# Optimization experiments

Measured on AMD Instinct MI355X. Metric: run time of the kernel, lower is better.

Reference implementation:

```python
import jax, jax.numpy as jnp
import numpy as np

T, B, X, F, Z, H = 64, 512, 784, 64, 64, 512


def _lin(v, W, b):
    return v @ W.T + b


def _gru(xt, h, Wih, Whh, bih, bhh):
    # PyTorch GRUCell gate math
    gi = xt @ Wih.T + bih
    gh = h @ Whh.T + bhh
    ir, iz, in_ = jnp.split(gi, 3, axis=-1)
    hr, hz, hn = jnp.split(gh, 3, axis=-1)
    r = jax.nn.sigmoid(ir + hr)
    z = jax.nn.sigmoid(iz + hz)
    n = jnp.tanh(in_ + r * hn)
    return (1.0 - z) * n + z * h


def _kld(mu1, sd1, mu2, sd2):
    r = sd1 / sd2
    return 0.5 * jnp.sum(((mu1 - mu2) / sd2) ** 2 + r ** 2 - 2.0 * jnp.log(r) - 1.0)


def setup_inputs() -> dict:
    key = jax.random.key(0)
    ks = iter(jax.random.split(key, 64))

    def Wn(*shape):
        return 0.02 * jax.random.normal(next(ks), shape, jnp.float32)

    d = {}
    d["x"] = jax.random.uniform(next(ks), (T, B, X), jnp.float32)
    d["eps_f"] = jax.random.normal(next(ks), (B, F), jnp.float32)
    d["eps_z"] = jax.random.normal(next(ks), (T, B, Z), jnp.float32)
    d.update(
        pxW1=Wn(H, X), pxb1=Wn(H), pxW2=Wn(H, H), pxb2=Wn(H),
        pzW=Wn(H, Z), pzb=Wn(H),
        pfW=Wn(H, F), pfb=Wn(H),
        rWih=Wn(3 * H, 3 * H), rWhh=Wn(3 * H, H), rbih=Wn(3 * H), rbhh=Wn(3 * H),
        zpW=Wn(H, H), zpb=Wn(H), zpmW=Wn(Z, H), zpmb=Wn(Z), zpsW=Wn(Z, H), zpsb=Wn(Z),
        feWih=Wn(3 * H, H), feWhh=Wn(3 * H, H), febih=Wn(3 * H), febhh=Wn(3 * H),
        femW=Wn(F, H), femb=Wn(F), fesW=Wn(F, H), fesb=Wn(F),
        zeW1=Wn(H, 2 * H), zeb1=Wn(H), zeW2=Wn(H, H), zeb2=Wn(H),
        zemW=Wn(Z, H), zemb=Wn(Z), zesW=Wn(Z, H), zesb=Wn(Z),
        dW1=Wn(H, 3 * H), db1=Wn(H), dW2=Wn(H, H), db2=Wn(H),
        dmW=Wn(X, H), dmb=Wn(X),
    )
    return d


def reference(x, eps_f, eps_z, pxW1, pxb1, pxW2, pxb2, pzW, pzb, pfW, pfb,
              rWih, rWhh, rbih, rbhh, zpW, zpb, zpmW, zpmb, zpsW, zpsb,
              feWih, feWhh, febih, febhh, femW, femb, fesW, fesb,
              zeW1, zeb1, zeW2, zeb2, zemW, zemb, zesW, zesb,
              dW1, db1, dW2, db2, dmW, dmb):
    relu = jax.nn.relu
    # phi_x over all timesteps at once: [T, B, H]
    phi_x = relu(_lin(relu(_lin(x, pxW1, pxb1)), pxW2, pxb2))
    h0 = jnp.zeros((x.shape[1], H), x.dtype)

    # f encoder GRU over the sequence; only the final hidden is used
    f_h, _ = jax.lax.scan(
        lambda h, xt: (_gru(xt, h, feWih, feWhh, febih, febhh), None), h0, phi_x)
    f_mean = _lin(f_h, femW, femb)
    f_std = jax.nn.softplus(_lin(f_h, fesW, fesb))
    f = eps_f * f_std + f_mean
    phi_f = relu(_lin(f, pfW, pfb))
    f_kld = _kld(f_mean, f_std, jnp.zeros_like(f_mean), jnp.ones_like(f_std))

    def step(carry, inp):
        h, zk, nll = carry
        px_t, e_t, x_t = inp
        zp = relu(_lin(h, zpW, zpb))
        zpm = _lin(zp, zpmW, zpmb)
        zps = jax.nn.softplus(_lin(zp, zpsW, zpsb))
        ze = relu(_lin(relu(_lin(jnp.concatenate([px_t, h], 1), zeW1, zeb1)), zeW2, zeb2))
        zem = _lin(ze, zemW, zemb)
        zes = jax.nn.softplus(_lin(ze, zesW, zesb))
        z_t = e_t * zes + zem
        phi_z = relu(_lin(z_t, pzW, pzb))
        dec = relu(_lin(relu(_lin(jnp.concatenate([phi_z, phi_f, h], 1), dW1, db1)), dW2, db2))
        dec_mean = jax.nn.sigmoid(_lin(dec, dmW, dmb))
        h_new = _gru(jnp.concatenate([px_t, phi_z, phi_f], 1), h, rWih, rWhh, rbih, rbhh)
        zk = zk + _kld(zem, zes, zpm, zps)
        nll = nll - jnp.sum(x_t * jnp.log(dec_mean) + (1.0 - x_t) * jnp.log(1.0 - dec_mean))
        return (h_new, zk, nll), None

    zero = jnp.zeros((), x.dtype)
    (_, z_kld, nll), _ = jax.lax.scan(step, (h0, zero, zero), (phi_x, eps_z, x))
    return (f_kld, z_kld, nll)
```

## Files before the change

### kernel.cpp

```cpp
#include <hip/hip_runtime.h>
#include <cmath>

namespace {

constexpr int Tn = 64;
constexpr int Bn = 512;
constexpr int Xn = 784;
constexpr int XnP = 800;
constexpr int Fn = 64;
constexpr int Zn = 64;
constexpr int Hn = 512;

typedef unsigned short us;
typedef __attribute__((ext_vector_type(8))) short bf16x8;
typedef __attribute__((ext_vector_type(4))) float f32x4;

__device__ __forceinline__ us f2b(float v) {
  unsigned int u = __float_as_uint(v);
  return (us)((u + 0x7FFFu + ((u >> 16) & 1u)) >> 16);
}
__device__ __forceinline__ float b2f(us u) { return __uint_as_float(((unsigned int)u) << 16); }
__device__ __forceinline__ float sigmf(float v) { return 1.0f / (1.0f + __expf(-v)); }
__device__ __forceinline__ float splusf(float v) {
  return v > 0.0f ? (v + log1pf(__expf(-v))) : log1pf(__expf(v));
}
__device__ __forceinline__ float block_sum(float v, float* red) {
  #pragma unroll
  for (int off = 32; off > 0; off >>= 1) v += __shfl_down(v, off, 64);
  if ((threadIdx.x & 63) == 0) red[threadIdx.x >> 6] = v;
  __syncthreads();
  float s = 0.0f;
  if (threadIdx.x == 0) s = red[0] + red[1] + red[2] + red[3];
  return s;
}

__global__ void cvt(const float* __restrict__ s, us* __restrict__ d, int n) {
  int i = blockIdx.x * 256 + threadIdx.x;
  if (i < n) d[i] = f2b(s[i]);
}
__global__ void cvt_pad(const float* __restrict__ s, us* __restrict__ d, int C, int Cp, int n) {
  int i = blockIdx.x * 256 + threadIdx.x;
  if (i < n) {
    int r = i / Cp, c = i - r * Cp;
    d[i] = (c < C) ? f2b(s[(size_t)r * C + c]) : (us)0;
  }
}

template <int NSEG, bool RELU, bool F32OUT, bool HASINIT, bool HASBIAS>
__device__ void tile_gemmx(
    int bx, int by,
    const us* A0, const us* W0, int ldw0, int K0,
    const us* A1, const us* W1, int ldw1, int K1,
    const float* initC, int ldi, const float* bias,
    void* Cout, int ldc, char* smemc)
{
  us* As = (us*)smemc; us* Bs = (us*)(smemc + 5120);
  const int tid = threadIdx.x, srow = tid >> 2, scb = (tid & 3) * 8;
  const int lane = tid & 63, w = tid >> 6, l15 = lane & 15, q = lane >> 4;
  const int m0 = by * 64, n0 = bx * 64;
  f32x4 acc[4];
  if (HASINIT) {
    #pragma unroll
    for (int j = 0; j < 4; ++j)
      #pragma unroll
      for (int r = 0; r < 4; ++r)
        acc[j][r] = initC[(size_t)(m0 + w * 16 + q * 4 + r) * ldi + n0 + j * 16 + l15];
  } else {
    #pragma unroll
    for (int j = 0; j < 4; ++j) acc[j] = (f32x4){0.f, 0.f, 0.f, 0.f};
  }
  #pragma unroll
  for (int seg = 0; seg < NSEG; ++seg) {
    const us* A = (seg == 0) ? A0 : A1;
    const us* W = (seg == 0) ? W0 : W1;
    const int ldw = (seg == 0) ? ldw0 : ldw1;
    const int K   = (seg == 0) ? K0 : K1;
    const us* ap = A + (size_t)(m0 + srow) * K + scb;
    const us* wp = W + (size_t)(n0 + srow) * ldw + scb;
    uint4 av = *(const uint4*)ap;
    uint4 wv = *(const uint4*)wp;
    for (int k0 = 0; k0 < K; k0 += 32) {
      __syncthreads();
      *(uint4*)&As[srow * 40 + scb] = av;
      *(uint4*)&Bs[srow * 40 + scb] = wv;
      __syncthreads();
      if (k0 + 32 < K) {
        av = *(const uint4*)(ap + k0 + 32);
        wv = *(const uint4*)(wp + k0 + 32);
      }
      bf16x8 a = *(const bf16x8*)&As[(w * 16 + l15) * 40 + q * 8];
      #pragma unroll
      for (int j = 0; j < 4; ++j) {
        bf16x8 b = *(const bf16x8*)&Bs[(j * 16 + l15) * 40 + q * 8];
        acc[j] = __builtin_amdgcn_mfma_f32_16x16x32_bf16(a, b, acc[j], 0, 0, 0);
      }
    }
  }
  #pragma unroll
  for (int j = 0; j < 4; ++j) {
    const int col = n0 + j * 16 + l15;
    const float bv = HASBIAS ? bias[col] : 0.f;
    #pragma unroll
    for (int r = 0; r < 4; ++r) {
      const int row = m0 + w * 16 + q * 4 + r;
      float v = acc[j][r] + bv;
      if (RELU) v = fmaxf(v, 0.f);
      if (F32OUT) ((float*)Cout)[(size_t)row * ldc + col] = v;
      else        ((us*)Cout)[(size_t)row * ldc + col] = f2b(v);
    }
  }
}

__device__ void tile_gru_fe(
    int bx, int by,
    const us* A0, const us* Wih,
    const us* hprev, const us* Whh,
    const float* bih, const float* bhh,
    us* hnew, char* smemc)
{
  us* Asm = (us*)smemc; us* Rs = (us*)(smemc + 5120);
  us* Zs = (us*)(smemc + 10240); us* Ns = (us*)(smemc + 15360);
  const int tid = threadIdx.x, srow = tid >> 2, scb = (tid & 3) * 8;
  const int lane = tid & 63, w = tid >> 6, l15 = lane & 15, q = lane >> 4;
  const int m0 = by * 64, c0 = bx * 64;
  f32x4 aR[4], aZ[4], aI[4], aH[4];
  #pragma unroll
  for (int j = 0; j < 4; ++j) {
    aR[j] = (f32x4){0.f, 0.f, 0.f, 0.f}; aZ[j] = aR[j]; aI[j] = aR[j]; aH[j] = aR[j];
  }
  #pragma unroll
  for (int seg = 0; seg < 2; ++seg) {
    const bool hseg = (seg == 1);
    const us* A  = hseg ? hprev : A0;
    const us* Wb = hseg ? Whh : Wih;
    const us* ap = A + (size_t)(m0 + srow) * Hn + scb;
    const us* wr = Wb + (size_t)(c0 + srow) * Hn + scb;
    const us* wz = wr + (size_t)Hn * Hn;
    const us* wn = wz + (size_t)Hn * Hn;
    uint4 av = *(const uint4*)ap;
    uint4 rv = *(const uint4*)wr;
    uint4 zv = *(const uint4*)wz;
    uint4 nv = *(const uint4*)wn;
    for (int k0 = 0; k0 < Hn; k0 += 32) {
      __syncthreads();
      *(uint4*)&Asm[srow * 40 + scb] = av;
      *(uint4*)&Rs[srow * 40 + scb] = rv;
      *(uint4*)&Zs[srow * 40 + scb] = zv;
      *(uint4*)&Ns[srow * 40 + scb] = nv;
      __syncthreads();
      if (k0 + 32 < Hn) {
        av = *(const uint4*)(ap + k0 + 32);
        rv = *(const uint4*)(wr + k0 + 32);
        zv = *(const uint4*)(wz + k0 + 32);
        nv = *(const uint4*)(wn + k0 + 32);
      }
      bf16x8 a = *(const bf16x8*)&Asm[(w * 16 + l15) * 40 + q * 8];
      #pragma unroll
      for (int j = 0; j < 4; ++j) {
        bf16x8 br = *(const bf16x8*)&Rs[(j * 16 + l15) * 40 + q * 8];
        bf16x8 bz = *(const bf16x8*)&Zs[(j * 16 + l15) * 40 + q * 8];
        bf16x8 bn = *(const bf16x8*)&Ns[(j * 16 + l15) * 40 + q * 8];
        aR[j] = __builtin_amdgcn_mfma_f32_16x16x32_bf16(a, br, aR[j], 0, 0, 0);
        aZ[j] = __builtin_amdgcn_mfma_f32_16x16x32_bf16(a, bz, aZ[j], 0, 0, 0);
        if (hseg) aH[j] = __builtin_amdgcn_mfma_f32_16x16x32_bf16(a, bn, aH[j], 0, 0, 0);
        else      aI[j] = __builtin_amdgcn_mfma_f32_16x16x32_bf16(a, bn, aI[j], 0, 0, 0);
      }
    }
  }
  #pragma unroll
  for (int j = 0; j < 4; ++j) {
    const int c = c0 + j * 16 + l15;
    const float bR = bih[c] + bhh[c];
    const float bZ = bih[Hn + c] + bhh[Hn + c];
    const float bI = bih[2 * Hn + c];
    const float bH = bhh[2 * Hn + c];
    #pragma unroll
    for (int r = 0; r < 4; ++r) {
      const int m = m0 + w * 16 + q * 4 + r;
      const float h = b2f(hprev[(size_t)m * Hn + c]);
      const float rg = sigmf(aR[j][r] + bR);
      const float zg = sigmf(aZ[j][r] + bZ);
      const float ng = tanhf(aI[j][r] + bI + rg * (aH[j][r] + bH));
      hnew[(size_t)m * Hn + c] = f2b((1.0f - zg) * ng + zg * h);
    }
  }
}

__device__ void tile_gru_fin(
    int bx, int by,
    const us* phiz, const us* rWih,
    const float* gipre, const float* ghpre,
    const us* hprev,
    const float* bih, const float* bhh,
    us* hnew, char* smemc)
{
  us* Asm = (us*)smemc; us* Rs = (us*)(smemc + 5120);
  us* Zs = (us*)(smemc + 10240); us* Ns = (us*)(smemc + 15360);
  const int tid = threadIdx.x, srow = tid >> 2, scb = (tid & 3) * 8;
  const int lane = tid & 63, w = tid >> 6, l15 = lane & 15, q = lane >> 4;
  const int m0 = by * 64, c0 = bx * 64;
  f32x4 aR[4], aZ[4], aI[4];
  float aH[4][4];
  #pragma unroll
  for (int j = 0; j < 4; ++j) {
    const int c = c0 + j * 16 + l15;
    #pragma unroll
    for (int r = 0; r < 4; ++r) {
      const size_t row = (size_t)(m0 + w * 16 + q * 4 + r) * 1536;
      aR[j][r] = gipre[row + c] + ghpre[row + c];
      aZ[j][r] = gipre[row + 512 + c] + ghpre[row + 512 + c];
      aI[j][r] = gipre[row + 1024 + c];
      aH[j][r] = ghpre[row + 1024 + c];
    }
  }
  const us* ap = phiz + (size_t)(m0 + srow) * Hn + scb;
  const us* wr = rWih + (size_t)(c0 + srow) * 1536 + 512 + scb;
  const us* wz = wr + (size_t)512 * 1536;
  const us* wn = wz + (size_t)512 * 1536;
  uint4 av = *(const uint4*)ap;
  uint4 rv = *(const uint4*)wr;
  uint4 zv = *(const uint4*)wz;
  uint4 nv = *(const uint4*)wn;
  for (int k0 = 0; k0 < Hn; k0 += 32) {
    __syncthreads();
    *(uint4*)&Asm[srow * 40 + scb] = av;
    *(uint4*)&Rs[srow * 40 + scb] = rv;
    *(uint4*)&Zs[srow * 40 + scb] = zv;
    *(uint4*)&Ns[srow * 40 + scb] = nv;
    __syncthreads();
    if (k0 + 32 < Hn) {
      av = *(const uint4*)(ap + k0 + 32);
      rv = *(const uint4*)(wr + k0 + 32);
      zv = *(const uint4*)(wz + k0 + 32);
      nv = *(const uint4*)(wn + k0 + 32);
    }
    bf16x8 a = *(const bf16x8*)&Asm[(w * 16 + l15) * 40 + q * 8];
    #pragma unroll
    for (int j = 0; j < 4; ++j) {
      bf16x8 br = *(const bf16x8*)&Rs[(j * 16 + l15) * 40 + q * 8];
      bf16x8 bz = *(const bf16x8*)&Zs[(j * 16 + l15) * 40 + q * 8];
      bf16x8 bn = *(const bf16x8*)&Ns[(j * 16 + l15) * 40 + q * 8];
      aR[j] = __builtin_amdgcn_mfma_f32_16x16x32_bf16(a, br, aR[j], 0, 0, 0);
      aZ[j] = __builtin_amdgcn_mfma_f32_16x16x32_bf16(a, bz, aZ[j], 0, 0, 0);
      aI[j] = __builtin_amdgcn_mfma_f32_16x16x32_bf16(a, bn, aI[j], 0, 0, 0);
    }
  }
  #pragma unroll
  for (int j = 0; j < 4; ++j) {
    const int c = c0 + j * 16 + l15;
    const float bR = bih[c] + bhh[c];
    const float bZ = bih[Hn + c] + bhh[Hn + c];
    const float bI = bih[2 * Hn + c];
    const float bH = bhh[2 * Hn + c];
    #pragma unroll
    for (int r = 0; r < 4; ++r) {
      const int m = m0 + w * 16 + q * 4 + r;
      const float h = b2f(hprev[(size_t)m * Hn + c]);
      const float rg = sigmf(aR[j][r] + bR);
      const float zg = sigmf(aZ[j][r] + bZ);
      const float ng = tanhf(aI[j][r] + bI + rg * (aH[j][r] + bH));
      hnew[(size_t)m * Hn + c] = f2b((1.0f - zg) * ng + zg * h);
    }
  }
}

__device__ void tile_nll(
    int bx, int by,
    const us* dec, const us* dmW, const float* dmb, const float* xt,
    float* nll, char* smemc)
{
  us* As = (us*)smemc; us* Bs = (us*)(smemc + 5120);
  float* red = (float*)(smemc + 10240);
  const int tid = threadIdx.x, srow = tid >> 2, scb = (tid & 3) * 8;
  const int lane = tid & 63, w = tid >> 6, l15 = lane & 15, q = lane >> 4;
  const int m0 = by * 64, n0 = bx * 64;
  f32x4 acc[4];
  #pragma unroll
  for (int j = 0; j < 4; ++j) acc[j] = (f32x4){0.f, 0.f, 0.f, 0.f};
  const int wrow = (n0 + srow < Xn) ? (n0 + srow) : (Xn - 1);
  const us* ap = dec + (size_t)(m0 + srow) * Hn + scb;
  const us* wp = dmW + (size_t)wrow * Hn + scb;
  uint4 av = *(const uint4*)ap;
  uint4 wv = *(const uint4*)wp;
  for (int k0 = 0; k0 < Hn; k0 += 32) {
    __syncthreads();
    *(uint4*)&As[srow * 40 + scb] = av;
    *(uint4*)&Bs[srow * 40 + scb] = wv;
    __syncthreads();
    if (k0 + 32 < Hn) {
      av = *(const uint4*)(ap + k0 + 32);
      wv = *(const uint4*)(wp + k0 + 32);
    }
    bf16x8 a = *(const bf16x8*)&As[(w * 16 + l15) * 40 + q * 8];
    #pragma unroll
    for (int j = 0; j < 4; ++j) {
      bf16x8 b = *(const bf16x8*)&Bs[(j * 16 + l15) * 40 + q * 8];
      acc[j] = __builtin_amdgcn_mfma_f32_16x16x32_bf16(a, b, acc[j], 0, 0, 0);
    }
  }
  float sum = 0.0f;
  #pragma unroll
  for (int j = 0; j < 4; ++j) {
    const int n = n0 + j * 16 + l15;
    if (n < Xn) {
      const float bv = dmb[n];
      #pragma unroll
      for (int r = 0; r < 4; ++r) {
        const int m = m0 + w * 16 + q * 4 + r;
        const float a = acc[j][r] + bv;
        const float xv = xt[(size_t)m * Xn + n];
        sum += splusf(-a) + (1.0f - xv) * a;
      }
    }
  }
  const float s = block_sum(sum, red);
  if (tid == 0) atomicAdd(nll, s);
}

template <int MODE>
__device__ void stat_dual(int vb,
    const us* Ain, const us* Wm, const float* bm, const us* Ws, const float* bs,
    const float* eps, const float* pm_in, const float* ps_in,
    us* o0b, float* o_pm, float* o_ps, float* kacc, char* smemc)
{
  us* As = (us*)smemc; us* Ms = (us*)(smemc + 5120); us* Ss = (us*)(smemc + 10240);
  float* red = (float*)(smemc + 15360);
  const int tid = threadIdx.x, srow = tid >> 2, scb = (tid & 3) * 8;
  const int lane = tid & 63, w = tid >> 6, l15 = lane & 15, q = lane >> 4;
  const int m0 = vb * 64;
  f32x4 am[4], as_[4];
  #pragma unroll
  for (int j = 0; j < 4; ++j) { am[j] = (f32x4){0.f, 0.f, 0.f, 0.f}; as_[j] = am[j]; }
  const us* ap = Ain + (size_t)(m0 + srow) * Hn + scb;
  const us* mp = Wm + (size_t)srow * Hn + scb;
  const us* sp = Ws + (size_t)srow * Hn + scb;
  uint4 av = *(const uint4*)ap;
  uint4 mv = *(const uint4*)mp;
  uint4 sv = *(const uint4*)sp;
  for (int k0 = 0; k0 < Hn; k0 += 32) {
    __syncthreads();
    *(uint4*)&As[srow * 40 + scb] = av;
    *(uint4*)&Ms[srow * 40 + scb] = mv;
    *(uint4*)&Ss[srow * 40 + scb] = sv;
    __syncthreads();
    if (k0 + 32 < Hn) {
      av = *(const uint4*)(ap + k0 + 32);
      mv = *(const uint4*)(mp + k0 + 32);
      sv = *(const uint4*)(sp + k0 + 32);
    }
    bf16x8 a = *(const bf16x8*)&As[(w * 16 + l15) * 40 + q * 8];
    #pragma unroll
    for (int j = 0; j < 4; ++j) {
      bf16x8 b0 = *(const bf16x8*)&Ms[(j * 16 + l15) * 40 + q * 8];
      bf16x8 b1 = *(const bf16x8*)&Ss[(j * 16 + l15) * 40 + q * 8];
      am[j]  = __builtin_amdgcn_mfma_f32_16x16x32_bf16(a, b0, am[j], 0, 0, 0);
      as_[j] = __builtin_amdgcn_mfma_f32_16x16x32_bf16(a, b1, as_[j], 0, 0, 0);
    }
  }
  float kld = 0.0f;
  #pragma unroll
  for (int j = 0; j < 4; ++j) {
    const int c = j * 16 + l15;
    const float bmv = bm[c], bsv = bs[c];
    #pragma unroll
    for (int r = 0; r < 4; ++r) {
      const int m = m0 + w * 16 + q * 4 + r;
      const float mu = am[j][r] + bmv;
      const float sd = splusf(as_[j][r] + bsv);
      if (MODE == 0) {
        o_pm[(size_t)m * Zn + c] = mu;
        o_ps[(size_t)m * Zn + c] = sd;
      } else {
        o0b[(size_t)m * Zn + c] = f2b(eps[(size_t)m * Zn + c] * sd + mu);
        if (MODE == 1) {
          kld += mu * mu + sd * sd - 2.0f * __logf(sd) - 1.0f;
        } else {
          const float pm = pm_in[(size_t)m * Zn + c];
          const float ps = ps_in[(size_t)m * Zn + c];
          const float dd = (mu - pm) / ps;
          const float rr = sd / ps;
          kld += dd * dd + rr * rr - 2.0f * __logf(rr) - 1.0f;
        }
      }
    }
  }
  if (MODE != 0) {
    const float s = block_sum(kld, red);
    if (tid == 0) atomicAdd(kacc, 0.5f * s);
  }
}

__global__ __launch_bounds__(256) void k_gemmA(
    const us* A, const us* W, int ldw, int K, const float* bias, us* C, int ldc)
{
  __shared__ alignas(16) char sm[10240];
  tile_gemmx<1, true, false, false, true>(blockIdx.x, blockIdx.y, A, W, ldw, K,
      nullptr, nullptr, 0, 0, nullptr, 0, bias, C, ldc, sm);
}

__global__ __launch_bounds__(256) void k_gruB(
    const us* A0, const us* Wih, const us* hprev, const us* Whh,
    const float* bih, const float* bhh, us* hnew)
{
  __shared__ alignas(16) char sm[20480];
  tile_gru_fe(blockIdx.x, blockIdx.y, A0, Wih, hprev, Whh, bih, bhh, hnew, sm);
}

__global__ __launch_bounds__(256) void k_statf(
    const us* fh, const us* femW, const float* femb, const us* fesW, const float* fesb,
    const float* eps_f, us* fbuf, float* kacc)
{
  __shared__ alignas(16) char sm[15376];
  stat_dual<1>(blockIdx.x, fh, femW, femb, fesW, fesb, eps_f,
               nullptr, nullptr, fbuf, nullptr, nullptr, kacc, sm);
}

__global__ __launch_bounds__(256) void kP2(
    const us* phi_f, const us* rWih, const us* dW1, const float* db1,
    float* Cpre_gru, float* Cpre_dec)
{
  __shared__ alignas(16) char sm[10240];
  const int b = blockIdx.x;
  if (b < 192)
    tile_gemmx<1, false, true, false, false>(b % 24, b / 24, phi_f, rWih + 1024, 1536, Hn,
        nullptr, nullptr, 0, 0, nullptr, 0, nullptr, Cpre_gru, 1536, sm);
  else
    tile_gemmx<1, false, true, false, true>((b - 192) & 7, (b - 192) >> 3,
        phi_f, dW1 + 512, 1536, Hn,
        nullptr, nullptr, 0, 0, nullptr, 0, db1, Cpre_dec, 512, sm);
}

__global__ __launch_bounds__(256) void kP3(
    const us* h0, const us* zpW, const float* zpb, us* zp,
    const us* px0, const us* zeW1, const float* zeb1, us* zepre)
{
  __shared__ alignas(16) char sm[10240];
  const int b = blockIdx.x;
  if (b < 64)
    tile_gemmx<1, true, false, false, true>(b & 7, b >> 3, h0, zpW, Hn, Hn,
        nullptr, nullptr, 0, 0, nullptr, 0, zpb, zp, Hn, sm);
  else
    tile_gemmx<2, true, false, false, true>((b - 64) & 7, (b - 64) >> 3,
        px0, zeW1, 1024, Hn, h0, zeW1 + 512, 1024, Hn,
        nullptr, 0, zeb1, zepre, Hn, sm);
}

__global__ __launch_bounds__(256) void kP4(
    const us* zepre, const us* zeW2, const float* zeb2, us* ze,
    const us* zp, const us* zpmW, const float* zpmb, const us* zpsW, const float* zpsb,
    float* zpm, float* zps)
{
  __shared__ alignas(16) char sm[15376];
  const int b = blockIdx.x;
  if (b < 64)
    tile_gemmx<1, true, false, false, true>(b & 7, b >> 3, zepre, zeW2, Hn, Hn,
        nullptr, nullptr, 0, 0, nullptr, 0, zeb2, ze, Hn, sm);
  else
    stat_dual<0>(b - 64, zp, zpmW, zpmb, zpsW, zpsb,
                 nullptr, nullptr, nullptr, nullptr, zpm, zps, nullptr, sm);
}

__global__ __launch_bounds__(256) void kS1(
    const us* ze, const us* zemW, const float* zemb, const us* zesW, const float* zesb,
    const float* eps_zt, const float* zpm, const float* zps, us* zt, float* kacc,
    const us* px_t, const us* rWih, const float* Cpre_gru, float* gipre)
{
  __shared__ alignas(16) char sm[15376];
  const int b = blockIdx.x;
  if (b < 8)
    stat_dual<2>(b, ze, zemW, zemb, zesW, zesb, eps_zt, zpm, zps,
                 zt, nullptr, nullptr, kacc, sm);
  else {
    const int tb = b - 8;
    tile_gemmx<1, false, true, true, false>(tb % 24, tb / 24, px_t, rWih, 1536, Hn,
        nullptr, nullptr, 0, 0, Cpre_gru, 1536, nullptr, gipre, 1536, sm);
  }
}

__global__ __launch_bounds__(256) void kS2(
    const us* zt, const us* pzW, const float* pzb, us* phiz)
{
  __shared__ alignas(16) char sm[10240];
  tile_gemmx<1, true, false, false, true>(blockIdx.x & 7, blockIdx.x >> 3, zt, pzW, Zn, Zn,
      nullptr, nullptr, 0, 0, nullptr, 0, pzb, phiz, Hn, sm);
}

__global__ __launch_bounds__(256) void kS3(
    const us* phiz, const us* rWih, const float* gipre, const float* ghpre,
    const us* hprev, const float* rbih, const float* rbhh, us* hnew,
    const us* dW1, const float* dtmph, us* dtmp)
{
  __shared__ alignas(16) char sm[20480];
  const int b = blockIdx.x;
  if (b < 64)
    tile_gru_fin(b & 7, b >> 3, phiz, rWih, gipre, ghpre, hprev, rbih, rbhh, hnew, sm);
  else
    tile_gemmx<1, true, false, true, false>((b - 64) & 7, (b - 64) >> 3, phiz, dW1, 1536, Hn,
        nullptr, nullptr, 0, 0, dtmph, 512, nullptr, dtmp, Hn, sm);
}

__global__ __launch_bounds__(256) void kS4(
    const us* dtmp, const us* dW2, const float* db2, us* dec,
    const us* hnext, const us* zpW, const float* zpb, us* zp,
    const us* px1, const us* zeW1, const float* zeb1, us* zepre,
    const us* dW1, const float* Cpre_dec, float* dtmph)
{
  __shared__ alignas(16) char sm[10240];
  const int b = blockIdx.x;
  if (b < 64)
    tile_gemmx<1, true, false, false, true>(b & 7, b >> 3, dtmp, dW2, Hn, Hn,
        nullptr, nullptr, 0, 0, nullptr, 0, db2, dec, Hn, sm);
  else if (b < 128)
    tile_gemmx<1, true, false, false, true>((b - 64) & 7, (b - 64) >> 3, hnext, zpW, Hn, Hn,
        nullptr, nullptr, 0, 0, nullptr, 0, zpb, zp, Hn, sm);
  else if (b < 192)
    tile_gemmx<2, true, false, false, true>((b - 128) & 7, (b - 128) >> 3,
        px1, zeW1, 1024, Hn, hnext, zeW1 + 512, 1024, Hn,
        nullptr, 0, zeb1, zepre, Hn, sm);
  else
    tile_gemmx<1, false, true, true, false>((b - 192) & 7, (b - 192) >> 3,
        hnext, dW1 + 1024, 1536, Hn,
        nullptr, nullptr, 0, 0, Cpre_dec, 512, nullptr, dtmph, 512, sm);
}

__global__ __launch_bounds__(256) void kS5(
    const us* dec, const us* dmW, const float* dmb, const float* xt, float* nll,
    const us* zepre, const us* zeW2, const float* zeb2, us* ze,
    const us* zp, const us* zpmW, const float* zpmb, const us* zpsW, const float* zpsb,
    float* zpm, float* zps,
    const us* hnext, const us* rWhh, float* ghpre)
{
  __shared__ alignas(16) char sm[15376];
  const int b = blockIdx.x;
  if (b < 104)
    tile_nll(b % 13, b / 13, dec, dmW, dmb, xt, nll, sm);
  else if (b < 168)
    tile_gemmx<1, true, false, false, true>((b - 104) & 7, (b - 104) >> 3, zepre, zeW2, Hn, Hn,
        nullptr, nullptr, 0, 0, nullptr, 0, zeb2, ze, Hn, sm);
  else if (b < 176)
    stat_dual<0>(b - 168, zp, zpmW, zpmb, zpsW, zpsb,
                 nullptr, nullptr, nullptr, nullptr, zpm, zps, nullptr, sm);
  else {
    const int tb = b - 176;
    tile_gemmx<1, false, true, false, false>(tb % 24, tb / 24, hnext, rWhh, Hn, Hn,
        nullptr, nullptr, 0, 0, nullptr, 0, nullptr, ghpre, 1536, sm);
  }
}

}

extern "C" void kernel_launch(void* const* d_in, const int* in_sizes, int n_in,
                              void* d_out, int out_size, void* d_ws, size_t ws_size,
                              hipStream_t stream)
{
  (void)in_sizes; (void)n_in; (void)out_size;
  const float* x     = (const float*)d_in[0];
  const float* eps_f = (const float*)d_in[1];
  const float* eps_z = (const float*)d_in[2];
  const float* pxW1  = (const float*)d_in[3];
  const float* pxb1  = (const float*)d_in[4];
  const float* pxW2  = (const float*)d_in[5];
  const float* pxb2  = (const float*)d_in[6];
  const float* pzW   = (const float*)d_in[7];
  const float* pzb   = (const float*)d_in[8];
  const float* pfW   = (const float*)d_in[9];
  const float* pfb   = (const float*)d_in[10];
  const float* rWih  = (const float*)d_in[11];
  const float* rWhh  = (const float*)d_in[12];
  const float* rbih  = (const float*)d_in[13];
  const float* rbhh  = (const float*)d_in[14];
  const float* zpW   = (const float*)d_in[15];
  const float* zpb   = (const float*)d_in[16];
  const float* zpmW  = (const float*)d_in[17];
  const float* zpmb  = (const float*)d_in[18];
  const float* zpsW  = (const float*)d_in[19];
  const float* zpsb  = (const float*)d_in[20];
  const float* feWih = (const float*)d_in[21];
  const float* feWhh = (const float*)d_in[22];
  const float* febih = (const float*)d_in[23];
  const float* febhh = (const float*)d_in[24];
  const float* femW  = (const float*)d_in[25];
  const float* femb  = (const float*)d_in[26];
  const float* fesW  = (const float*)d_in[27];
  const float* fesb  = (const float*)d_in[28];
  const float* zeW1  = (const float*)d_in[29];
  const float* zeb1  = (const float*)d_in[30];
  const float* zeW2  = (const float*)d_in[31];
  const float* zeb2  = (const float*)d_in[32];
  const float* zemW  = (const float*)d_in[33];
  const float* zemb  = (const float*)d_in[34];
  const float* zesW  = (const float*)d_in[35];
  const float* zesb  = (const float*)d_in[36];
  const float* dW1   = (const float*)d_in[37];
  const float* db1   = (const float*)d_in[38];
  const float* dW2   = (const float*)d_in[39];
  const float* db2   = (const float*)d_in[40];
  const float* dmW   = (const float*)d_in[41];
  const float* dmb   = (const float*)d_in[42];
  float* out = (float*)d_out;

  char* base = (char*)d_ws;
  size_t off = 0;
  auto ab = [&](size_t bytes) -> void* {
    void* p = base + off;
    off += (bytes + 255) & ~(size_t)255;
    return p;
  };

  us* b_pxW1  = (us*)ab((size_t)512 * XnP * 2);
  us* b_pxW2  = (us*)ab((size_t)512 * 512 * 2);
  us* b_pzW   = (us*)ab((size_t)512 * 64 * 2);
  us* b_pfW   = (us*)ab((size_t)512 * 64 * 2);
  us* b_rWih  = (us*)ab((size_t)1536 * 1536 * 2);
  us* b_rWhh  = (us*)ab((size_t)1536 * 512 * 2);
  us* b_zpW   = (us*)ab((size_t)512 * 512 * 2);
  us* b_zpmW  = (us*)ab((size_t)64 * 512 * 2);
  us* b_zpsW  = (us*)ab((size_t)64 * 512 * 2);
  us* b_feWih = (us*)ab((size_t)1536 * 512 * 2);
  us* b_feWhh = (us*)ab((size_t)1536 * 512 * 2);
  us* b_femW  = (us*)ab((size_t)64 * 512 * 2);
  us* b_fesW  = (us*)ab((size_t)64 * 512 * 2);
  us* b_zeW1  = (us*)ab((size_t)512 * 1024 * 2);
  us* b_zeW2  = (us*)ab((size_t)512 * 512 * 2);
  us* b_zemW  = (us*)ab((size_t)64 * 512 * 2);
  us* b_zesW  = (us*)ab((size_t)64 * 512 * 2);
  us* b_dW1   = (us*)ab((size_t)512 * 1536 * 2);
  us* b_dW2   = (us*)ab((size_t)512 * 512 * 2);
  us* b_dmW   = (us*)ab((size_t)Xn * 512 * 2);

  us* phi_x = (us*)ab((size_t)Tn * Bn * Hn * 2);
  us* fh_a  = (us*)ab((size_t)Bn * Hn * 2);
  us* h_a   = (us*)ab((size_t)Bn * Hn * 2);
  us* fh_b  = (us*)ab((size_t)Bn * Hn * 2);
  us* h_b   = (us*)ab((size_t)Bn * Hn * 2);
  us* fbuf  = (us*)ab((size_t)Bn * Fn * 2);
  us* phi_f = (us*)ab((size_t)Bn * Hn * 2);
  us* zp    = (us*)ab((size_t)Bn * Hn * 2);
  us* zepre = (us*)ab((size_t)Bn * Hn * 2);
  us* ze    = (us*)ab((size_t)Bn * Hn * 2);
  us* zt    = (us*)ab((size_t)Bn * Zn * 2);
  us* phiz  = (us*)ab((size_t)Bn * Hn * 2);
  us* dtmp  = (us*)ab((size_t)Bn * Hn * 2);
  us* dec   = (us*)ab((size_t)Bn * Hn * 2);
  float* zpm = (float*)ab((size_t)Bn * Zn * 4);
  float* zps = (float*)ab((size_t)Bn * Zn * 4);
  float* Cpre_gru = (float*)ab((size_t)Bn * 1536 * 4);
  float* Cpre_dec = (float*)ab((size_t)Bn * 512 * 4);
  float* gipre    = (float*)ab((size_t)Bn * 1536 * 4);
  float* ghpre    = (float*)ab((size_t)Bn * 1536 * 4);
  float* dtmph    = (float*)ab((size_t)Bn * 512 * 4);

  int CH = 16;
  while (CH > 1 && off + (size_t)CH * (Bn * XnP + Bn * Hn) * 2 + 4096 > ws_size) CH >>= 1;
  us* xch  = (us*)ab((size_t)CH * Bn * XnP * 2);
  us* tmpb = (us*)ab((size_t)CH * Bn * Hn * 2);

  hipMemsetAsync(d_out, 0, 3 * sizeof(float), stream);
  hipMemsetAsync(fh_a, 0, 2 * (size_t)Bn * Hn * 2, stream);
  hipMemsetAsync(ghpre, 0, (size_t)Bn * 1536 * 4, stream);

  const dim3 blk(256);
  auto CVT = [&](const float* s, us* d, size_t n) {
    cvt<<<dim3((unsigned)((n + 255) / 256)), blk, 0, stream>>>(s, d, (int)n);
  };

  {
    const size_t n = (size_t)512 * XnP;
    cvt_pad<<<dim3((unsigned)((n + 255) / 256)), blk, 0, stream>>>(pxW1, b_pxW1, Xn, XnP, (int)n);
  }
  CVT(pxW2, b_pxW2, (size_t)512 * 512);
  CVT(pzW, b_pzW, (size_t)512 * 64);
  CVT(pfW, b_pfW, (size_t)512 * 64);
  CVT(rWih, b_rWih, (size_t)1536 * 1536);
  CVT(rWhh, b_rWhh, (size_t)1536 * 512);
  CVT(zpW, b_zpW, (size_t)512 * 512);
  CVT(zpmW, b_zpmW, (size_t)64 * 512);
  CVT(zpsW, b_zpsW, (size_t)64 * 512);
  CVT(feWih, b_feWih, (size_t)1536 * 512);
  CVT(feWhh, b_feWhh, (size_t)1536 * 512);
  CVT(femW, b_femW, (size_t)64 * 512);
  CVT(fesW, b_fesW, (size_t)64 * 512);
  CVT(zeW1, b_zeW1, (size_t)512 * 1024);
  CVT(zeW2, b_zeW2, (size_t)512 * 512);
  CVT(zemW, b_zemW, (size_t)64 * 512);
  CVT(zesW, b_zesW, (size_t)64 * 512);
  CVT(dW1, b_dW1, (size_t)512 * 1536);
  CVT(dW2, b_dW2, (size_t)512 * 512);
  CVT(dmW, b_dmW, (size_t)Xn * 512);

  for (int c = 0; c < Tn / CH; ++c) {
    const size_t nx = (size_t)CH * Bn * XnP;
    cvt_pad<<<dim3((unsigned)((nx + 255) / 256)), blk, 0, stream>>>(
        x + (size_t)c * CH * Bn * Xn, xch, Xn, XnP, (int)nx);
    const dim3 gA(8, CH * Bn / 64);
    k_gemmA<<<gA, blk, 0, stream>>>(xch, b_pxW1, XnP, XnP, pxb1, tmpb, Hn);
    k_gemmA<<<gA, blk, 0, stream>>>(tmpb, b_pxW2, Hn, Hn, pxb2,
                                    phi_x + (size_t)c * CH * Bn * Hn, Hn);
  }

  us* fc = fh_a; us* fn2 = fh_b;
  for (int t = 0; t < Tn; ++t) {
    k_gruB<<<dim3(8, 8), blk, 0, stream>>>(
        phi_x + (size_t)t * Bn * Hn, b_feWih, fc, b_feWhh, febih, febhh, fn2);
    us* sw = fc; fc = fn2; fn2 = sw;
  }

  k_statf<<<dim3(8), blk, 0, stream>>>(fh_a, b_femW, femb, b_fesW, fesb, eps_f, fbuf, out + 0);

  k_gemmA<<<dim3(8, 8), blk, 0, stream>>>(fbuf, b_pfW, Fn, Fn, pfb, phi_f, Hn);
  kP2<<<dim3(256), blk, 0, stream>>>(phi_f, b_rWih, b_dW1, db1, Cpre_gru, Cpre_dec);
  hipMemcpyAsync(dtmph, Cpre_dec, (size_t)Bn * 512 * 4, hipMemcpyDeviceToDevice, stream);
  kP3<<<dim3(128), blk, 0, stream>>>(h_a, b_zpW, zpb, zp, phi_x, b_zeW1, zeb1, zepre);
  kP4<<<dim3(72), blk, 0, stream>>>(zepre, b_zeW2, zeb2, ze,
                                    zp, b_zpmW, zpmb, b_zpsW, zpsb, zpm, zps);

  for (int t = 0; t < Tn; ++t) {
    const us* hcur = (t & 1) ? h_b : h_a;
    us* hnext      = (t & 1) ? h_a : h_b;
    const bool last = (t == Tn - 1);
    const us* px_t = phi_x + (size_t)t * Bn * Hn;

    kS1<<<dim3(200), blk, 0, stream>>>(
        ze, b_zemW, zemb, b_zesW, zesb, eps_z + (size_t)t * Bn * Zn, zpm, zps,
        zt, out + 1, px_t, b_rWih, Cpre_gru, gipre);

    kS2<<<dim3(64), blk, 0, stream>>>(zt, b_pzW, pzb, phiz);

    kS3<<<dim3(128), blk, 0, stream>>>(
        phiz, b_rWih, gipre, ghpre, hcur, rbih, rbhh, hnext,
        b_dW1, dtmph, dtmp);

    kS4<<<dim3(last ? 64 : 256), blk, 0, stream>>>(
        dtmp, b_dW2, db2, dec,
        hnext, b_zpW, zpb, zp,
        phi_x + (size_t)(t + 1) * Bn * Hn, b_zeW1, zeb1, zepre,
        b_dW1, Cpre_dec, dtmph);

    kS5<<<dim3(last ? 104 : 368), blk, 0, stream>>>(
        dec, b_dmW, dmb, x + (size_t)t * Bn * Xn, out + 2,
        zepre, b_zeW2, zeb2, ze,
        zp, b_zpmW, zpmb, b_zpsW, zpsb, zpm, zps,
        hnext, b_rWhh, ghpre);
  }
}
```

Baseline: 6.581 ms.

## Double-buffer LDS in GEMM tiles, fuse x conversion and phiz into stats kernel

Converts every MFMA tile loop (generic GEMM, GRU tiles, NLL, stat tiles) to double-buffered shared memory with one barrier per k-step instead of two. The phi_x first layer now reads fp32 x directly and converts to bf16 in-register, removing the separate padding conversion pass and chunked loop. The phi_z projection is fused into the per-step stats kernel, which drops one launch per timestep, and the prologue kernels P2/P3 are merged while an initial device copy is replaced by pointer selection. In exchange it doubles LDS usage per block, which may reduce occupancy, and it allocates a full-sequence intermediate buffer.

```diff
diff --git a/kernel.cpp b/kernel.cpp
--- a/kernel.cpp
+++ b/kernel.cpp
@@ -54,7 +54,6 @@
     const float* initC, int ldi, const float* bias,
     void* Cout, int ldc, char* smemc)
 {
-  us* As = (us*)smemc; us* Bs = (us*)(smemc + 5120);
   const int tid = threadIdx.x, srow = tid >> 2, scb = (tid & 3) * 8;
   const int lane = tid & 63, w = tid >> 6, l15 = lane & 15, q = lane >> 4;
   const int m0 = by * 64, n0 = bx * 64;
@@ -69,32 +68,41 @@
     #pragma unroll
     for (int j = 0; j < 4; ++j) acc[j] = (f32x4){0.f, 0.f, 0.f, 0.f};
   }
-  #pragma unroll
-  for (int seg = 0; seg < NSEG; ++seg) {
-    const us* A = (seg == 0) ? A0 : A1;
-    const us* W = (seg == 0) ? W0 : W1;
-    const int ldw = (seg == 0) ? ldw0 : ldw1;
-    const int K   = (seg == 0) ? K0 : K1;
-    const us* ap = A + (size_t)(m0 + srow) * K + scb;
-    const us* wp = W + (size_t)(n0 + srow) * ldw + scb;
-    uint4 av = *(const uint4*)ap;
-    uint4 wv = *(const uint4*)wp;
-    for (int k0 = 0; k0 < K; k0 += 32) {
-      __syncthreads();
-      *(uint4*)&As[srow * 40 + scb] = av;
-      *(uint4*)&Bs[srow * 40 + scb] = wv;
-      __syncthreads();
-      if (k0 + 32 < K) {
-        av = *(const uint4*)(ap + k0 + 32);
-        wv = *(const uint4*)(wp + k0 + 32);
-      }
-      bf16x8 a = *(const bf16x8*)&As[(w * 16 + l15) * 40 + q * 8];
-      #pragma unroll
-      for (int j = 0; j < 4; ++j) {
-        bf16x8 b = *(const bf16x8*)&Bs[(j * 16 + l15) * 40 + q * 8];
-        acc[j] = __builtin_amdgcn_mfma_f32_16x16x32_bf16(a, b, acc[j], 0, 0, 0);
-      }
-    }
+  const int nt0 = K0 / 32;
+  const int nt = (NSEG == 2) ? nt0 + K1 / 32 : nt0;
+  auto ld = [&](int kt, uint4& av, uint4& wv) {
+    if (NSEG == 2 && kt >= nt0) {
+      const int k = (kt - nt0) * 32;
+      av = *(const uint4*)(A1 + (size_t)(m0 + srow) * K1 + k + scb);
+      wv = *(const uint4*)(W1 + (size_t)(n0 + srow) * ldw1 + k + scb);
+    } else {
+      const int k = kt * 32;
+      av = *(const uint4*)(A0 + (size_t)(m0 + srow) * K0 + k + scb);
+      wv = *(const uint4*)(W0 + (size_t)(n0 + srow) * ldw0 + k + scb);
+    }
+  };
+  uint4 av, wv;
+  ld(0, av, wv);
+  *(uint4*)&((us*)smemc)[srow * 40 + scb] = av;
+  *(uint4*)&((us*)(smemc + 5120))[srow * 40 + scb] = wv;
+  __syncthreads();
+  for (int kt = 0; kt < nt; ++kt) {
+    const int cur = kt & 1;
+    us* Asc = (us*)(smemc + cur * 10240);
+    us* Bsc = (us*)(smemc + cur * 10240 + 5120);
+    const bool more = (kt + 1 < nt);
+    if (more) ld(kt + 1, av, wv);
+    bf16x8 a = *(const bf16x8*)&Asc[(w * 16 + l15) * 40 + q * 8];
+    #pragma unroll
+    for (int j = 0; j < 4; ++j) {
+      bf16x8 b = *(const bf16x8*)&Bsc[(j * 16 + l15) * 40 + q * 8];
+      acc[j] = __builtin_amdgcn_mfma_f32_16x16x32_bf16(a, b, acc[j], 0, 0, 0);
+    }
+    if (more) {
+      *(uint4*)&((us*)(smemc + (cur ^ 1) * 10240))[srow * 40 + scb] = av;
+      *(uint4*)&((us*)(smemc + (cur ^ 1) * 10240 + 5120))[srow * 40 + scb] = wv;
+    }
+    __syncthreads();
   }
   #pragma unroll
   for (int j = 0; j < 4; ++j) {
@@ -111,15 +119,71 @@
   }
 }
 
+__device__ void tile_gA1(int bx, int by, const float* __restrict__ X, const us* W,
+                         const float* bias, us* C, char* smemc)
+{
+  const int tid = threadIdx.x, srow = tid >> 2, scb = (tid & 3) * 8;
+  const int lane = tid & 63, w = tid >> 6, l15 = lane & 15, q = lane >> 4;
+  const int m0 = by * 64, n0 = bx * 64;
+  f32x4 acc[4];
+  #pragma unroll
+  for (int j = 0; j < 4; ++j) acc[j] = (f32x4){0.f, 0.f, 0.f, 0.f};
+  auto ldA = [&](int k) -> uint4 {
+    if (k + scb < Xn) {
+      const float* p = X + (size_t)(m0 + srow) * Xn + k + scb;
+      float4 f0 = *(const float4*)p;
+      float4 f1 = *(const float4*)(p + 4);
+      union { us h[8]; uint4 u; } pk;
+      pk.h[0] = f2b(f0.x); pk.h[1] = f2b(f0.y); pk.h[2] = f2b(f0.z); pk.h[3] = f2b(f0.w);
+      pk.h[4] = f2b(f1.x); pk.h[5] = f2b(f1.y); pk.h[6] = f2b(f1.z); pk.h[7] = f2b(f1.w);
+      return pk.u;
+    }
+    return (uint4){0, 0, 0, 0};
+  };
+  const int nt = XnP / 32;
+  uint4 av = ldA(0);
+  uint4 wv = *(const uint4*)(W + (size_t)(n0 + srow) * XnP + scb);
+  *(uint4*)&((us*)smemc)[srow * 40 + scb] = av;
+  *(uint4*)&((us*)(smemc + 5120))[srow * 40 + scb] = wv;
+  __syncthreads();
+  for (int kt = 0; kt < nt; ++kt) {
+    const int cur = kt & 1;
+    us* Asc = (us*)(smemc + cur * 10240);
+    us* Bsc = (us*)(smemc + cur * 10240 + 5120);
+    const bool more = (kt + 1 < nt);
+    if (more) {
+      av = ldA((kt + 1) * 32);
+      wv = *(const uint4*)(W + (size_t)(n0 + srow) * XnP + (kt + 1) * 32 + scb);
+    }
+    bf16x8 a = *(const bf16x8*)&Asc[(w * 16 + l15) * 40 + q * 8];
+    #pragma unroll
+    for (int j = 0; j < 4; ++j) {
+      bf16x8 b = *(const bf16x8*)&Bsc[(j * 16 + l15) * 40 + q * 8];
+      acc[j] = __builtin_amdgcn_mfma_f32_16x16x32_bf16(a, b, acc[j], 0, 0, 0);
+    }
+    if (more) {
+      *(uint4*)&((us*)(smemc + (cur ^ 1) * 10240))[srow * 40 + scb] = av;
+      *(uint4*)&((us*)(smemc + (cur ^ 1) * 10240 + 5120))[srow * 40 + scb] = wv;
+    }
+    __syncthreads();
+  }
+  #pragma unroll
+  for (int j = 0; j < 4; ++j) {
+    const int col = n0 + j * 16 + l15;
+    const float bv = bias[col];
+    #pragma unroll
+    for (int r = 0; r < 4; ++r) {
+      const int row = m0 + w * 16 + q * 4 + r;
+      C[(size_t)row * Hn + col] = f2b(fmaxf(acc[j][r] + bv, 0.f));
+    }
+  }
+}
+
 __device__ void tile_gru_fe(
-    int bx, int by,
-    const us* A0, const us* Wih,
+    int bx, int by, const us* A0, const us* Wih,
     const us* hprev, const us* Whh,
-    const float* bih, const float* bhh,
-    us* hnew, char* smemc)
-{
-  us* Asm = (us*)smemc; us* Rs = (us*)(smemc + 5120);
-  us* Zs = (us*)(smemc + 10240); us* Ns = (us*)(smemc + 15360);
+    const float* bih, const float* bhh, us* hnew, char* smemc)
+{
   const int tid = threadIdx.x, srow = tid >> 2, scb = (tid & 3) * 8;
   const int lane = tid & 63, w = tid >> 6, l15 = lane & 15, q = lane >> 4;
   const int m0 = by * 64, c0 = bx * 64;
@@ -128,44 +192,49 @@
   for (int j = 0; j < 4; ++j) {
     aR[j] = (f32x4){0.f, 0.f, 0.f, 0.f}; aZ[j] = aR[j]; aI[j] = aR[j]; aH[j] = aR[j];
   }
-  #pragma unroll
-  for (int seg = 0; seg < 2; ++seg) {
-    const bool hseg = (seg == 1);
+  auto ld = [&](int kt, uint4& av, uint4& rv, uint4& zv, uint4& nv) {
+    const bool hseg = kt >= 16;
     const us* A  = hseg ? hprev : A0;
     const us* Wb = hseg ? Whh : Wih;
-    const us* ap = A + (size_t)(m0 + srow) * Hn + scb;
-    const us* wr = Wb + (size_t)(c0 + srow) * Hn + scb;
-    const us* wz = wr + (size_t)Hn * Hn;
-    const us* wn = wz + (size_t)Hn * Hn;
-    uint4 av = *(const uint4*)ap;
-    uint4 rv = *(const uint4*)wr;
-    uint4 zv = *(const uint4*)wz;
-    uint4 nv = *(const uint4*)wn;
-    for (int k0 = 0; k0 < Hn; k0 += 32) {
-      __syncthreads();
-      *(uint4*)&Asm[srow * 40 + scb] = av;
-      *(uint4*)&Rs[srow * 40 + scb] = rv;
-      *(uint4*)&Zs[srow * 40 + scb] = zv;
-      *(uint4*)&Ns[srow * 40 + scb] = nv;
-      __syncthreads();
-      if (k0 + 32 < Hn) {
-        av = *(const uint4*)(ap + k0 + 32);
-        rv = *(const uint4*)(wr + k0 + 32);
-        zv = *(const uint4*)(wz + k0 + 32);
-        nv = *(const uint4*)(wn + k0 + 32);
-      }
-      bf16x8 a = *(const bf16x8*)&Asm[(w * 16 + l15) * 40 + q * 8];
-      #pragma unroll
-      for (int j = 0; j < 4; ++j) {
-        bf16x8 br = *(const bf16x8*)&Rs[(j * 16 + l15) * 40 + q * 8];
-        bf16x8 bz = *(const bf16x8*)&Zs[(j * 16 + l15) * 40 + q * 8];
-        bf16x8 bn = *(const bf16x8*)&Ns[(j * 16 + l15) * 40 + q * 8];
-        aR[j] = __builtin_amdgcn_mfma_f32_16x16x32_bf16(a, br, aR[j], 0, 0, 0);
-        aZ[j] = __builtin_amdgcn_mfma_f32_16x16x32_bf16(a, bz, aZ[j], 0, 0, 0);
-        if (hseg) aH[j] = __builtin_amdgcn_mfma_f32_16x16x32_bf16(a, bn, aH[j], 0, 0, 0);
-        else      aI[j] = __builtin_amdgcn_mfma_f32_16x16x32_bf16(a, bn, aI[j], 0, 0, 0);
-      }
-    }
+    const int k = (kt & 15) * 32;
+    av = *(const uint4*)(A + (size_t)(m0 + srow) * Hn + k + scb);
+    const us* wr = Wb + (size_t)(c0 + srow) * Hn + k + scb;
+    rv = *(const uint4*)wr;
+    zv = *(const uint4*)(wr + 262144);
+    nv = *(const uint4*)(wr + 524288);
+  };
+  uint4 av, rv, zv, nv;
+  ld(0, av, rv, zv, nv);
+  *(uint4*)&((us*)smemc)[srow * 40 + scb] = av;
+  *(uint4*)&((us*)(smemc + 5120))[srow * 40 + scb] = rv;
+  *(uint4*)&((us*)(smemc + 10240))[srow * 40 + scb] = zv;
+  *(uint4*)&((us*)(smemc + 15360))[srow * 40 + scb] = nv;
+  __syncthreads();
+  for (int kt = 0; kt < 32; ++kt) {
+    const int cur = kt & 1;
+    char* base = smemc + cur * 20480;
+    const bool hseg = kt >= 16;
+    const bool more = (kt + 1 < 32);
+    if (more) ld(kt + 1, av, rv, zv, nv);
+    bf16x8 a = *(const bf16x8*)&((us*)base)[(w * 16 + l15) * 40 + q * 8];
+    #pragma unroll
+    for (int j = 0; j < 4; ++j) {
+      bf16x8 br = *(const bf16x8*)&((us*)(base + 5120))[(j * 16 + l15) * 40 + q * 8];
+      bf16x8 bz = *(const bf16x8*)&((us*)(base + 10240))[(j * 16 + l15) * 40 + q * 8];
+      bf16x8 bn = *(const bf16x8*)&((us*)(base + 15360))[(j * 16 + l15) * 40 + q * 8];
+      aR[j] = __builtin_amdgcn_mfma_f32_16x16x32_bf16(a, br, aR[j], 0, 0, 0);
+      aZ[j] = __builtin_amdgcn_mfma_f32_16x16x32_bf16(a, bz, aZ[j], 0, 0, 0);
+      if (hseg) aH[j] = __builtin_amdgcn_mfma_f32_16x16x32_bf16(a, bn, aH[j], 0, 0, 0);
+      else      aI[j] = __builtin_amdgcn_mfma_f32_16x16x32_bf16(a, bn, aI[j], 0, 0, 0);
+    }
+    if (more) {
+      char* nb = smemc + (cur ^ 1) * 20480;
+      *(uint4*)&((us*)nb)[srow * 40 + scb] = av;
+      *(uint4*)&((us*)(nb + 5120))[srow * 40 + scb] = rv;
+      *(uint4*)&((us*)(nb + 10240))[srow * 40 + scb] = zv;
+      *(uint4*)&((us*)(nb + 15360))[srow * 40 + scb] = nv;
+    }
+    __syncthreads();
   }
   #pragma unroll
   for (int j = 0; j < 4; ++j) {
@@ -187,15 +256,10 @@
 }
 
 __device__ void tile_gru_fin(
-    int bx, int by,
-    const us* phiz, const us* rWih,
-    const float* gipre, const float* ghpre,
-    const us* hprev,
-    const float* bih, const float* bhh,
-    us* hnew, char* smemc)
-{
-  us* Asm = (us*)smemc; us* Rs = (us*)(smemc + 5120);
-  us* Zs = (us*)(smemc + 10240); us* Ns = (us*)(smemc + 15360);
+    int bx, int by, const us* phiz, const us* rWih,
+    const float* gipre, const float* ghpre, const us* hprev,
+    const float* bih, const float* bhh, us* hnew, char* smemc)
+{
   const int tid = threadIdx.x, srow = tid >> 2, scb = (tid & 3) * 8;
   const int lane = tid & 63, w = tid >> 6, l15 = lane & 15, q = lane >> 4;
   const int m0 = by * 64, c0 = bx * 64;
@@ -213,37 +277,44 @@
       aH[j][r] = ghpre[row + 1024 + c];
     }
   }
-  const us* ap = phiz + (size_t)(m0 + srow) * Hn + scb;
-  const us* wr = rWih + (size_t)(c0 + srow) * 1536 + 512 + scb;
-  const us* wz = wr + (size_t)512 * 1536;
-  const us* wn = wz + (size_t)512 * 1536;
-  uint4 av = *(const uint4*)ap;
-  uint4 rv = *(const uint4*)wr;
-  uint4 zv = *(const uint4*)wz;
-  uint4 nv = *(const uint4*)wn;
-  for (int k0 = 0; k0 < Hn; k0 += 32) {
-    __syncthreads();
-    *(uint4*)&Asm[srow * 40 + scb] = av;
-    *(uint4*)&Rs[srow * 40 + scb] = rv;
-    *(uint4*)&Zs[srow * 40 + scb] = zv;
-    *(uint4*)&Ns[srow * 40 + scb] = nv;
-    __syncthreads();
-    if (k0 + 32 < Hn) {
-      av = *(const uint4*)(ap + k0 + 32);
-      rv = *(const uint4*)(wr + k0 + 32);
-      zv = *(const uint4*)(wz + k0 + 32);
-      nv = *(const uint4*)(wn + k0 + 32);
-    }
-    bf16x8 a = *(const bf16x8*)&Asm[(w * 16 + l15) * 40 + q * 8];
+  auto ld = [&](int kt, uint4& av, uint4& rv, uint4& zv, uint4& nv) {
+    const int k = kt * 32;
+    av = *(const uint4*)(phiz + (size_t)(m0 + srow) * Hn + k + scb);
+    const us* wr = rWih + (size_t)(c0 + srow) * 1536 + 512 + k + scb;
+    rv = *(const uint4*)wr;
+    zv = *(const uint4*)(wr + 786432);
+    nv = *(const uint4*)(wr + 1572864);
+  };
+  uint4 av, rv, zv, nv;
+  ld(0, av, rv, zv, nv);
+  *(uint4*)&((us*)smemc)[srow * 40 + scb] = av;
+  *(uint4*)&((us*)(smemc + 5120))[srow * 40 + scb] = rv;
+  *(uint4*)&((us*)(smemc + 10240))[srow * 40 + scb] = zv;
+  *(uint4*)&((us*)(smemc + 15360))[srow * 40 + scb] = nv;
+  __syncthreads();
+  for (int kt = 0; kt < 16; ++kt) {
+    const int cur = kt & 1;
+    char* base = smemc + cur * 20480;
+    const bool more = (kt + 1 < 16);
+    if (more) ld(kt + 1, av, rv, zv, nv);
+    bf16x8 a = *(const bf16x8*)&((us*)base)[(w * 16 + l15) * 40 + q * 8];
     #pragma unroll
     for (int j = 0; j < 4; ++j) {
-      bf16x8 br = *(const bf16x8*)&Rs[(j * 16 + l15) * 40 + q * 8];
-      bf16x8 bz = *(const bf16x8*)&Zs[(j * 16 + l15) * 40 + q * 8];
-      bf16x8 bn = *(const bf16x8*)&Ns[(j * 16 + l15) * 40 + q * 8];
+      bf16x8 br = *(const bf16x8*)&((us*)(base + 5120))[(j * 16 + l15) * 40 + q * 8];
+      bf16x8 bz = *(const bf16x8*)&((us*)(base + 10240))[(j * 16 + l15) * 40 + q * 8];
+      bf16x8 bn = *(const bf16x8*)&((us*)(base + 15360))[(j * 16 + l15) * 40 + q * 8];
       aR[j] = __builtin_amdgcn_mfma_f32_16x16x32_bf16(a, br, aR[j], 0, 0, 0);
       aZ[j] = __builtin_amdgcn_mfma_f32_16x16x32_bf16(a, bz, aZ[j], 0, 0, 0);
       aI[j] = __builtin_amdgcn_mfma_f32_16x16x32_bf16(a, bn, aI[j], 0, 0, 0);
     }
+    if (more) {
+      char* nb = smemc + (cur ^ 1) * 20480;
+      *(uint4*)&((us*)nb)[srow * 40 + scb] = av;
+      *(uint4*)&((us*)(nb + 5120))[srow * 40 + scb] = rv;
+      *(uint4*)&((us*)(nb + 10240))[srow * 40 + scb] = zv;
+      *(uint4*)&((us*)(nb + 15360))[srow * 40 + scb] = nv;
+    }
+    __syncthreads();
   }
   #pragma unroll
   for (int j = 0; j < 4; ++j) {
@@ -265,12 +336,10 @@
 }
 
 __device__ void tile_nll(
-    int bx, int by,
-    const us* dec, const us* dmW, const float* dmb, const float* xt,
-    float* nll, char* smemc)
-{
-  us* As = (us*)smemc; us* Bs = (us*)(smemc + 5120);
-  float* red = (float*)(smemc + 10240);
+    int bx, int by, const us* dec, const us* dmW, const float* dmb,
+    const float* xt, float* nll, char* smemc)
+{
+  float* red = (float*)(smemc + 20480);
   const int tid = threadIdx.x, srow = tid >> 2, scb = (tid & 3) * 8;
   const int lane = tid & 63, w = tid >> 6, l15 = lane & 15, q = lane >> 4;
   const int m0 = by * 64, n0 = bx * 64;
@@ -282,21 +351,29 @@
   const us* wp = dmW + (size_t)wrow * Hn + scb;
   uint4 av = *(const uint4*)ap;
   uint4 wv = *(const uint4*)wp;
-  for (int k0 = 0; k0 < Hn; k0 += 32) {
+  *(uint4*)&((us*)smemc)[srow * 40 + scb] = av;
+  *(uint4*)&((us*)(smemc + 5120))[srow * 40 + scb] = wv;
+  __syncthreads();
+  for (int kt = 0; kt < 16; ++kt) {
+    const int cur = kt & 1;
+    us* Asc = (us*)(smemc + cur * 10240);
+    us* Bsc = (us*)(smemc + cur * 10240 + 5120);
+    const bool more = (kt + 1 < 16);
+    if (more) {
+      av = *(const uint4*)(ap + (kt + 1) * 32);
+      wv = *(const uint4*)(wp + (kt + 1) * 32);
+    }
+    bf16x8 a = *(const bf16x8*)&Asc[(w * 16 + l15) * 40 + q * 8];
+    #pragma unroll
+    for (int j = 0; j < 4; ++j) {
+      bf16x8 b = *(const bf16x8*)&Bsc[(j * 16 + l15) * 40 + q * 8];
+      acc[j] = __builtin_amdgcn_mfma_f32_16x16x32_bf16(a, b, acc[j], 0, 0, 0);
+    }
+    if (more) {
+      *(uint4*)&((us*)(smemc + (cur ^ 1) * 10240))[srow * 40 + scb] = av;
+      *(uint4*)&((us*)(smemc + (cur ^ 1) * 10240 + 5120))[srow * 40 + scb] = wv;
+    }
     __syncthreads();
-    *(uint4*)&As[srow * 40 + scb] = av;
-    *(uint4*)&Bs[srow * 40 + scb] = wv;
-    __syncthreads();
-    if (k0 + 32 < Hn) {
-      av = *(const uint4*)(ap + k0 + 32);
-      wv = *(const uint4*)(wp + k0 + 32);
-    }
-    bf16x8 a = *(const bf16x8*)&As[(w * 16 + l15) * 40 + q * 8];
-    #pragma unroll
-    for (int j = 0; j < 4; ++j) {
-      bf16x8 b = *(const bf16x8*)&Bs[(j * 16 + l15) * 40 + q * 8];
-      acc[j] = __builtin_amdgcn_mfma_f32_16x16x32_bf16(a, b, acc[j], 0, 0, 0);
-    }
   }
   float sum = 0.0f;
   #pragma unroll
@@ -320,11 +397,9 @@
 template <int MODE>
 __device__ void stat_dual(int vb,
     const us* Ain, const us* Wm, const float* bm, const us* Ws, const float* bs,
-    const float* eps, const float* pm_in, const float* ps_in,
-    us* o0b, float* o_pm, float* o_ps, float* kacc, char* smemc)
-{
-  us* As = (us*)smemc; us* Ms = (us*)(smemc + 5120); us* Ss = (us*)(smemc + 10240);
-  float* red = (float*)(smemc + 15360);
+    const float* eps, us* o0b, float* o_pm, float* o_ps, float* kacc, char* smemc)
+{
+  float* red = (float*)(smemc + 30720);
   const int tid = threadIdx.x, srow = tid >> 2, scb = (tid & 3) * 8;
   const int lane = tid & 63, w = tid >> 6, l15 = lane & 15, q = lane >> 4;
   const int m0 = vb * 64;
@@ -337,25 +412,34 @@
   uint4 av = *(const uint4*)ap;
   uint4 mv = *(const uint4*)mp;
   uint4 sv = *(const uint4*)sp;
-  for (int k0 = 0; k0 < Hn; k0 += 32) {
-    __syncthreads();
-    *(uint4*)&As[srow * 40 + scb] = av;
-    *(uint4*)&Ms[srow * 40 + scb] = mv;
-    *(uint4*)&Ss[srow * 40 + scb] = sv;
-    __syncthreads();
-    if (k0 + 32 < Hn) {
-      av = *(const uint4*)(ap + k0 + 32);
-      mv = *(const uint4*)(mp + k0 + 32);
-      sv = *(const uint4*)(sp + k0 + 32);
-    }
-    bf16x8 a = *(const bf16x8*)&As[(w * 16 + l15) * 40 + q * 8];
+  *(uint4*)&((us*)smemc)[srow * 40 + scb] = av;
+  *(uint4*)&((us*)(smemc + 5120))[srow * 40 + scb] = mv;
+  *(uint4*)&((us*)(smemc + 10240))[srow * 40 + scb] = sv;
+  __syncthreads();
+  for (int kt = 0; kt < 16; ++kt) {
+    const int cur = kt & 1;
+    char* base = smemc + cur * 15360;
+    const bool more = (kt + 1 < 16);
+    if (more) {
+      av = *(const uint4*)(ap + (kt + 1) * 32);
+      mv = *(const uint4*)(mp + (kt + 1) * 32);
+      sv = *(const uint4*)(sp + (kt + 1) * 32);
+    }
+    bf16x8 a = *(const bf16x8*)&((us*)base)[(w * 16 + l15) * 40 + q * 8];
     #pragma unroll
     for (int j = 0; j < 4; ++j) {
-      bf16x8 b0 = *(const bf16x8*)&Ms[(j * 16 + l15) * 40 + q * 8];
-      bf16x8 b1 = *(const bf16x8*)&Ss[(j * 16 + l15) * 40 + q * 8];
+      bf16x8 b0 = *(const bf16x8*)&((us*)(base + 5120))[(j * 16 + l15) * 40 + q * 8];
+      bf16x8 b1 = *(const bf16x8*)&((us*)(base + 10240))[(j * 16 + l15) * 40 + q * 8];
       am[j]  = __builtin_amdgcn_mfma_f32_16x16x32_bf16(a, b0, am[j], 0, 0, 0);
       as_[j] = __builtin_amdgcn_mfma_f32_16x16x32_bf16(a, b1, as_[j], 0, 0, 0);
     }
+    if (more) {
+      char* nb = smemc + ((cur ^ 1) * 15360);
+      *(uint4*)&((us*)nb)[srow * 40 + scb] = av;
+      *(uint4*)&((us*)(nb + 5120))[srow * 40 + scb] = mv;
+      *(uint4*)&((us*)(nb + 10240))[srow * 40 + scb] = sv;
+    }
+    __syncthreads();
   }
   float kld = 0.0f;
   #pragma unroll
@@ -372,15 +456,7 @@
         o_ps[(size_t)m * Zn + c] = sd;
       } else {
         o0b[(size_t)m * Zn + c] = f2b(eps[(size_t)m * Zn + c] * sd + mu);
-        if (MODE == 1) {
-          kld += mu * mu + sd * sd - 2.0f * __logf(sd) - 1.0f;
-        } else {
-          const float pm = pm_in[(size_t)m * Zn + c];
-          const float ps = ps_in[(size_t)m * Zn + c];
-          const float dd = (mu - pm) / ps;
-          const float rr = sd / ps;
-          kld += dd * dd + rr * rr - 2.0f * __logf(rr) - 1.0f;
-        }
+        kld += mu * mu + sd * sd - 2.0f * __logf(sd) - 1.0f;
       }
     }
   }
@@ -390,86 +466,188 @@
   }
 }
 
-__global__ __launch_bounds__(256) void k_gemmA(
+__device__ void statphiz(int vb,
+    const us* ze, const us* Wm, const float* bm, const us* Ws, const float* bs,
+    const float* eps, const float* zpm, const float* zps,
+    const us* pzW, const float* pzb, us* phiz, float* kacc, char* smemc)
+{
+  us* ztL = (us*)(smemc + 30720);
+  float* red = (float*)(smemc + 39936);
+  const int tid = threadIdx.x, srow = tid >> 2, scb = (tid & 3) * 8;
+  const int lane = tid & 63, w = tid >> 6, l15 = lane & 15, q = lane >> 4;
+  const int m0 = vb * 64;
+  f32x4 am[4], as_[4];
+  #pragma unroll
+  for (int j = 0; j < 4; ++j) { am[j] = (f32x4){0.f, 0.f, 0.f, 0.f}; as_[j] = am[j]; }
+  const us* ap = ze + (size_t)(m0 + srow) * Hn + scb;
+  const us* mp = Wm + (size_t)srow * Hn + scb;
+  const us* sp = Ws + (size_t)srow * Hn + scb;
+  uint4 av = *(const uint4*)ap;
+  uint4 mv = *(const uint4*)mp;
+  uint4 sv = *(const uint4*)sp;
+  *(uint4*)&((us*)smemc)[srow * 40 + scb] = av;
+  *(uint4*)&((us*)(smemc + 5120))[srow * 40 + scb] = mv;
+  *(uint4*)&((us*)(smemc + 10240))[srow * 40 + scb] = sv;
+  __syncthreads();
+  for (int kt = 0; kt < 16; ++kt) {
+    const int cur = kt & 1;
+    char* base = smemc + cur * 15360;
+    const bool more = (kt + 1 < 16);
+    if (more) {
+      av = *(const uint4*)(ap + (kt + 1) * 32);
+      mv = *(const uint4*)(mp + (kt + 1) * 32);
+      sv = *(const uint4*)(sp + (kt + 1) * 32);
+    }
+    bf16x8 a = *(const bf16x8*)&((us*)base)[(w * 16 + l15) * 40 + q * 8];
+    #pragma unroll
+    for (int j = 0; j < 4; ++j) {
+      bf16x8 b0 = *(const bf16x8*)&((us*)(base + 5120))[(j * 16 + l15) * 40 + q * 8];
+      bf16x8 b1 = *(const bf16x8*)&((us*)(base + 10240))[(j * 16 + l15) * 40 + q * 8];
+      am[j]  = __builtin_amdgcn_mfma_f32_16x16x32_bf16(a, b0, am[j], 0, 0, 0);
+      as_[j] = __builtin_amdgcn_mfma_f32_16x16x32_bf16(a, b1, as_[j], 0, 0, 0);
+    }
+    if (more) {
+      char* nb = smemc + ((cur ^ 1) * 15360);
+      *(uint4*)&((us*)nb)[srow * 40 + scb] = av;
+      *(uint4*)&((us*)(nb + 5120))[srow * 40 + scb] = mv;
+      *(uint4*)&((us*)(nb + 10240))[srow * 40 + scb] = sv;
+    }
+    __syncthreads();
+  }
+  float kld = 0.0f;
+  #pragma unroll
+  for (int j = 0; j < 4; ++j) {
+    const int c = j * 16 + l15;
+    const float bmv = bm[c], bsv = bs[c];
+    #pragma unroll
+    for (int r = 0; r < 4; ++r) {
+      const int row = w * 16 + q * 4 + r;
+      const int m = m0 + row;
+      const float mu = am[j][r] + bmv;
+      const float sd = splusf(as_[j][r] + bsv);
+      ztL[row * 72 + c] = f2b(eps[(size_t)m * Zn + c] * sd + mu);
+      const float pm = zpm[(size_t)m * Zn + c];
+      const float ps = zps[(size_t)m * Zn + c];
+      const float dd = (mu - pm) / ps;
+      const float rr = sd / ps;
+      kld += dd * dd + rr * rr - 2.0f * __logf(rr) - 1.0f;
+    }
+  }
+  const float s = block_sum(kld, red);
+  if (tid == 0) atomicAdd(kacc, 0.5f * s);
+  us* G = (us*)smemc;
+  for (int cc = 0; cc < 8; ++cc) {
+    f32x4 acc[4];
+    #pragma unroll
+    for (int j = 0; j < 4; ++j) acc[j] = (f32x4){0.f, 0.f, 0.f, 0.f};
+    #pragma unroll
+    for (int k0 = 0; k0 < 64; k0 += 32) {
+      uint4 wv = *(const uint4*)(pzW + (size_t)(cc * 64 + srow) * 64 + k0 + scb);
+      __syncthreads();
+      *(uint4*)&G[srow * 40 + scb] = wv;
+      __syncthreads();
+      bf16x8 a = *(const bf16x8*)&ztL[(w * 16 + l15) * 72 + k0 + q * 8];
+      #pragma unroll
+      for (int j = 0; j < 4; ++j) {
+        bf16x8 b = *(const bf16x8*)&G[(j * 16 + l15) * 40 + q * 8];
+        acc[j] = __builtin_amdgcn_mfma_f32_16x16x32_bf16(a, b, acc[j], 0, 0, 0);
+      }
+    }
+    #pragma unroll
+    for (int j = 0; j < 4; ++j) {
+      const int col = cc * 64 + j * 16 + l15;
+      const float bz = pzb[col];
+      #pragma unroll
+      for (int r = 0; r < 4; ++r) {
+        const int row = w * 16 + q * 4 + r;
+        phiz[(size_t)(m0 + row) * Hn + col] = f2b(fmaxf(acc[j][r] + bz, 0.f));
+      }
+    }
+  }
+}
+
+__global__ __launch_bounds__(256) void g_A1(
+    const float* X, const us* W, const float* bias, us* C)
+{
+  __shared__ alignas(16) char sm[20480];
+  tile_gA1(blockIdx.x, blockIdx.y, X, W, bias, C, sm);
+}
+
+__global__ __launch_bounds__(256) void g_gemm(
     const us* A, const us* W, int ldw, int K, const float* bias, us* C, int ldc)
 {
-  __shared__ alignas(16) char sm[10240];
+  __shared__ alignas(16) char sm[20480];
   tile_gemmx<1, true, false, false, true>(blockIdx.x, blockIdx.y, A, W, ldw, K,
       nullptr, nullptr, 0, 0, nullptr, 0, bias, C, ldc, sm);
 }
 
-__global__ __launch_bounds__(256) void k_gruB(
+__global__ __launch_bounds__(256) void g_gruB(
     const us* A0, const us* Wih, const us* hprev, const us* Whh,
     const float* bih, const float* bhh, us* hnew)
 {
-  __shared__ alignas(16) char sm[20480];
+  __shared__ alignas(16) char sm[40960];
   tile_gru_fe(blockIdx.x, blockIdx.y, A0, Wih, hprev, Whh, bih, bhh, hnew, sm);
 }
 
-__global__ __launch_bounds__(256) void k_statf(
+__global__ __launch_bounds__(256) void g_statf(
     const us* fh, const us* femW, const float* femb, const us* fesW, const float* fesb,
     const float* eps_f, us* fbuf, float* kacc)
 {
-  __shared__ alignas(16) char sm[15376];
+  __shared__ alignas(16) char sm[30736];
   stat_dual<1>(blockIdx.x, fh, femW, femb, fesW, fesb, eps_f,
-               nullptr, nullptr, fbuf, nullptr, nullptr, kacc, sm);
-}
-
-__global__ __launch_bounds__(256) void kP2(
+               fbuf, nullptr, nullptr, kacc, sm);
+}
+
+__global__ __launch_bounds__(256) void g_P23(
     const us* phi_f, const us* rWih, const us* dW1, const float* db1,
-    float* Cpre_gru, float* Cpre_dec)
-{
-  __shared__ alignas(16) char sm[10240];
+    float* Cpre_gru, float* Cpre_dec,
+    const us* h0, const us* zpW, const float* zpb, us* zp,
+    const us* px0, const us* zeW1, const float* zeb1, us* zepre)
+{
+  __shared__ alignas(16) char sm[20480];
   const int b = blockIdx.x;
   if (b < 192)
     tile_gemmx<1, false, true, false, false>(b % 24, b / 24, phi_f, rWih + 1024, 1536, Hn,
         nullptr, nullptr, 0, 0, nullptr, 0, nullptr, Cpre_gru, 1536, sm);
-  else
+  else if (b < 256)
     tile_gemmx<1, false, true, false, true>((b - 192) & 7, (b - 192) >> 3,
-        phi_f, dW1 + 512, 1536, Hn,
-        nullptr, nullptr, 0, 0, nullptr, 0, db1, Cpre_dec, 512, sm);
-}
-
-__global__ __launch_bounds__(256) void kP3(
-    const us* h0, const us* zpW, const float* zpb, us* zp,
-    const us* px0, const us* zeW1, const float* zeb1, us* zepre)
-{
-  __shared__ alignas(16) char sm[10240];
-  const int b = blockIdx.x;
-  if (b < 64)
-    tile_gemmx<1, true, false, false, true>(b & 7, b >> 3, h0, zpW, Hn, Hn,
+        phi_f, dW1 + 512, 1536, Hn, nullptr, nullptr, 0, 0,
+        nullptr, 0, db1, Cpre_dec, 512, sm);
+  else if (b < 320)
+    tile_gemmx<1, true, false, false, true>((b - 256) & 7, (b - 256) >> 3, h0, zpW, Hn, Hn,
         nullptr, nullptr, 0, 0, nullptr, 0, zpb, zp, Hn, sm);
   else
-    tile_gemmx<2, true, false, false, true>((b - 64) & 7, (b - 64) >> 3,
+    tile_gemmx<2, true, false, false, true>((b - 320) & 7, (b - 320) >> 3,
         px0, zeW1, 1024, Hn, h0, zeW1 + 512, 1024, Hn,
         nullptr, 0, zeb1, zepre, Hn, sm);
 }
 
-__global__ __launch_bounds__(256) void kP4(
+__global__ __launch_bounds__(256) void g_P4(
     const us* zepre, const us* zeW2, const float* zeb2, us* ze,
     const us* zp, const us* zpmW, const float* zpmb, const us* zpsW, const float* zpsb,
     float* zpm, float* zps)
 {
-  __shared__ alignas(16) char sm[15376];
+  __shared__ alignas(16) char sm[30736];
   const int b = blockIdx.x;
   if (b < 64)
     tile_gemmx<1, true, false, false, true>(b & 7, b >> 3, zepre, zeW2, Hn, Hn,
         nullptr, nullptr, 0, 0, nullptr, 0, zeb2, ze, Hn, sm);
   else
     stat_dual<0>(b - 64, zp, zpmW, zpmb, zpsW, zpsb,
-                 nullptr, nullptr, nullptr, nullptr, zpm, zps, nullptr, sm);
-}
-
-__global__ __launch_bounds__(256) void kS1(
+                 nullptr, nullptr, zpm, zps, nullptr, sm);
+}
+
+__global__ __launch_bounds__(256) void g_A(
     const us* ze, const us* zemW, const float* zemb, const us* zesW, const float* zesb,
-    const float* eps_zt, const float* zpm, const float* zps, us* zt, float* kacc,
+    const float* eps_zt, const float* zpm, const float* zps,
+    const us* pzW, const float* pzb, us* phiz, float* kacc,
     const us* px_t, const us* rWih, const float* Cpre_gru, float* gipre)
 {
-  __shared__ alignas(16) char sm[15376];
+  __shared__ alignas(16) char sm[40960];
   const int b = blockIdx.x;
   if (b < 8)
-    stat_dual<2>(b, ze, zemW, zemb, zesW, zesb, eps_zt, zpm, zps,
-                 zt, nullptr, nullptr, kacc, sm);
+    statphiz(b, ze, zemW, zemb, zesW, zesb, eps_zt, zpm, zps,
+             pzW, pzb, phiz, kacc, sm);
   else {
     const int tb = b - 8;
     tile_gemmx<1, false, true, true, false>(tb % 24, tb / 24, px_t, rWih, 1536, Hn,
@@ -477,20 +655,12 @@
   }
 }
 
-__global__ __launch_bounds__(256) void kS2(
-    const us* zt, const us* pzW, const float* pzb, us* phiz)
-{
-  __shared__ alignas(16) char sm[10240];
-  tile_gemmx<1, true, false, false, true>(blockIdx.x & 7, blockIdx.x >> 3, zt, pzW, Zn, Zn,
-      nullptr, nullptr, 0, 0, nullptr, 0, pzb, phiz, Hn, sm);
-}
-
-__global__ __launch_bounds__(256) void kS3(
+__global__ __launch_bounds__(256) void g_B(
     const us* phiz, const us* rWih, const float* gipre, const float* ghpre,
     const us* hprev, const float* rbih, const float* rbhh, us* hnew,
     const us* dW1, const float* dtmph, us* dtmp)
 {
-  __shared__ alignas(16) char sm[20480];
+  __shared__ alignas(16) char sm[40960];
   const int b = blockIdx.x;
   if (b < 64)
     tile_gru_fin(b & 7, b >> 3, phiz, rWih, gipre, ghpre, hprev, rbih, rbhh, hnew, sm);
@@ -499,13 +669,13 @@
         nullptr, nullptr, 0, 0, dtmph, 512, nullptr, dtmp, Hn, sm);
 }
 
-__global__ __launch_bounds__(256) void kS4(
+__global__ __launch_bounds__(256) void g_C(
     const us* dtmp, const us* dW2, const float* db2, us* dec,
     const us* hnext, const us* zpW, const float* zpb, us* zp,
     const us* px1, const us* zeW1, const float* zeb1, us* zepre,
     const us* dW1, const float* Cpre_dec, float* dtmph)
 {
-  __shared__ alignas(16) char sm[10240];
+  __shared__ alignas(16) char sm[20480];
   const int b = blockIdx.x;
   if (b < 64)
     tile_gemmx<1, true, false, false, true>(b & 7, b >> 3, dtmp, dW2, Hn, Hn,
@@ -519,18 +689,18 @@
         nullptr, 0, zeb1, zepre, Hn, sm);
   else
     tile_gemmx<1, false, true, true, false>((b - 192) & 7, (b - 192) >> 3,
-        hnext, dW1 + 1024, 1536, Hn,
-        nullptr, nullptr, 0, 0, Cpre_dec, 512, nullptr, dtmph, 512, sm);
-}
-
-__global__ __launch_bounds__(256) void kS5(
+        hnext, dW1 + 1024, 1536, Hn, nullptr, nullptr, 0, 0,
+        Cpre_dec, 512, nullptr, dtmph, 512, sm);
+}
+
+__global__ __launch_bounds__(256) void g_D(
     const us* dec, const us* dmW, const float* dmb, const float* xt, float* nll,
     const us* zepre, const us* zeW2, const float* zeb2, us* ze,
     const us* zp, const us* zpmW, const float* zpmb, const us* zpsW, const float* zpsb,
     float* zpm, float* zps,
     const us* hnext, const us* rWhh, float* ghpre)
 {
-  __shared__ alignas(16) char sm[15376];
+  __shared__ alignas(16) char sm[30736];
   const int b = blockIdx.x;
   if (b < 104)
     tile_nll(b % 13, b / 13, dec, dmW, dmb, xt, nll, sm);
@@ -539,7 +709,7 @@
         nullptr, nullptr, 0, 0, nullptr, 0, zeb2, ze, Hn, sm);
   else if (b < 176)
     stat_dual<0>(b - 168, zp, zpmW, zpmb, zpsW, zpsb,
-                 nullptr, nullptr, nullptr, nullptr, zpm, zps, nullptr, sm);
+                 nullptr, nullptr, zpm, zps, nullptr, sm);
   else {
     const int tb = b - 176;
     tile_gemmx<1, false, true, false, false>(tb % 24, tb / 24, hnext, rWhh, Hn, Hn,
@@ -553,7 +723,7 @@
                               void* d_out, int out_size, void* d_ws, size_t ws_size,
                               hipStream_t stream)
 {
-  (void)in_sizes; (void)n_in; (void)out_size;
+  (void)in_sizes; (void)n_in; (void)out_size; (void)ws_size;
   const float* x     = (const float*)d_in[0];
   const float* eps_f = (const float*)d_in[1];
   const float* eps_z = (const float*)d_in[2];
@@ -629,6 +799,7 @@
   us* b_dmW   = (us*)ab((size_t)Xn * 512 * 2);
 
   us* phi_x = (us*)ab((size_t)Tn * Bn * Hn * 2);
+  us* tmpA  = (us*)ab((size_t)Tn * Bn * Hn * 2);
   us* fh_a  = (us*)ab((size_t)Bn * Hn * 2);
   us* h_a   = (us*)ab((size_t)Bn * Hn * 2);
   us* fh_b  = (us*)ab((size_t)Bn * Hn * 2);
@@ -638,7 +809,6 @@
   us* zp    = (us*)ab((size_t)Bn * Hn * 2);
   us* zepre = (us*)ab((size_t)Bn * Hn * 2);
   us* ze    = (us*)ab((size_t)Bn * Hn * 2);
-  us* zt    = (us*)ab((size_t)Bn * Zn * 2);
   us* phiz  = (us*)ab((size_t)Bn * Hn * 2);
   us* dtmp  = (us*)ab((size_t)Bn * Hn * 2);
   us* dec   = (us*)ab((size_t)Bn * Hn * 2);
@@ -649,11 +819,6 @@
   float* gipre    = (float*)ab((size_t)Bn * 1536 * 4);
   float* ghpre    = (float*)ab((size_t)Bn * 1536 * 4);
   float* dtmph    = (float*)ab((size_t)Bn * 512 * 4);
-
-  int CH = 16;
-  while (CH > 1 && off + (size_t)CH * (Bn * XnP + Bn * Hn) * 2 + 4096 > ws_size) CH >>= 1;
-  us* xch  = (us*)ab((size_t)CH * Bn * XnP * 2);
-  us* tmpb = (us*)ab((size_t)CH * Bn * Hn * 2);
 
   hipMemsetAsync(d_out, 0, 3 * sizeof(float), stream);
   hipMemsetAsync(fh_a, 0, 2 * (size_t)Bn * Hn * 2, stream);
@@ -688,55 +853,45 @@
   CVT(dW2, b_dW2, (size_t)512 * 512);
   CVT(dmW, b_dmW, (size_t)Xn * 512);
 
-  for (int c = 0; c < Tn / CH; ++c) {
-    const size_t nx = (size_t)CH * Bn * XnP;
-    cvt_pad<<<dim3((unsigned)((nx + 255) / 256)), blk, 0, stream>>>(
-        x + (size_t)c * CH * Bn * Xn, xch, Xn, XnP, (int)nx);
-    const dim3 gA(8, CH * Bn / 64);
-    k_gemmA<<<gA, blk, 0, stream>>>(xch, b_pxW1, XnP, XnP, pxb1, tmpb, Hn);
-    k_gemmA<<<gA, blk, 0, stream>>>(tmpb, b_pxW2, Hn, Hn, pxb2,
-                                    phi_x + (size_t)c * CH * Bn * Hn, Hn);
-  }
+  g_A1<<<dim3(8, Tn * Bn / 64), blk, 0, stream>>>(x, b_pxW1, pxb1, tmpA);
+  g_gemm<<<dim3(8, Tn * Bn / 64), blk, 0, stream>>>(tmpA, b_pxW2, Hn, Hn, pxb2, phi_x, Hn);
 
   us* fc = fh_a; us* fn2 = fh_b;
   for (int t = 0; t < Tn; ++t) {
-    k_gruB<<<dim3(8, 8), blk, 0, stream>>>(
+    g_gruB<<<dim3(8, 8), blk, 0, stream>>>(
         phi_x + (size_t)t * Bn * Hn, b_feWih, fc, b_feWhh, febih, febhh, fn2);
     us* sw = fc; fc = fn2; fn2 = sw;
   }
 
-  k_statf<<<dim3(8), blk, 0, stream>>>(fh_a, b_femW, femb, b_fesW, fesb, eps_f, fbuf, out + 0);
-
-  k_gemmA<<<dim3(8, 8), blk, 0, stream>>>(fbuf, b_pfW, Fn, Fn, pfb, phi_f, Hn);
-  kP2<<<dim3(256), blk, 0, stream>>>(phi_f, b_rWih, b_dW1, db1, Cpre_gru, Cpre_dec);
-  hipMemcpyAsync(dtmph, Cpre_dec, (size_t)Bn * 512 * 4, hipMemcpyDeviceToDevice, stream);
-  kP3<<<dim3(128), blk, 0, stream>>>(h_a, b_zpW, zpb, zp, phi_x, b_zeW1, zeb1, zepre);
-  kP4<<<dim3(72), blk, 0, stream>>>(zepre, b_zeW2, zeb2, ze,
-                                    zp, b_zpmW, zpmb, b_zpsW, zpsb, zpm, zps);
+  g_statf<<<dim3(8), blk, 0, stream>>>(fh_a, b_femW, femb, b_fesW, fesb, eps_f, fbuf, out + 0);
+
+  g_gemm<<<dim3(8, 8), blk, 0, stream>>>(fbuf, b_pfW, Fn, Fn, pfb, phi_f, Hn);
+  g_P23<<<dim3(384), blk, 0, stream>>>(phi_f, b_rWih, b_dW1, db1, Cpre_gru, Cpre_dec,
+                                       h_a, b_zpW, zpb, zp, phi_x, b_zeW1, zeb1, zepre);
+  g_P4<<<dim3(72), blk, 0, stream>>>(zepre, b_zeW2, zeb2, ze,
+                                     zp, b_zpmW, zpmb, b_zpsW, zpsb, zpm, zps);
 
   for (int t = 0; t < Tn; ++t) {
     const us* hcur = (t & 1) ? h_b : h_a;
     us* hnext      = (t & 1) ? h_a : h_b;
     const bool last = (t == Tn - 1);
     const us* px_t = phi_x + (size_t)t * Bn * Hn;
-
-    kS1<<<dim3(200), blk, 0, stream>>>(
+    const float* dtmph_sel = (t == 0) ? Cpre_dec : dtmph;
+
+    g_A<<<dim3(200), blk, 0, stream>>>(
         ze, b_zemW, zemb, b_zesW, zesb, eps_z + (size_t)t * Bn * Zn, zpm, zps,
-        zt, out + 1, px_t, b_rWih, Cpre_gru, gipre);
-
-    kS2<<<dim3(64), blk, 0, stream>>>(zt, b_pzW, pzb, phiz);
-
-    kS3<<<dim3(128), blk, 0, stream>>>(
+        b_pzW, pzb, phiz, out + 1, px_t, b_rWih, Cpre_gru, gipre);
+
+    g_B<<<dim3(128), blk, 0, stream>>>(
         phiz, b_rWih, gipre, ghpre, hcur, rbih, rbhh, hnext,
-        b_dW1, dtmph, dtmp);
-
-    kS4<<<dim3(last ? 64 : 256), blk, 0, stream>>>(
-        dtmp, b_dW2, db2, dec,
-        hnext, b_zpW, zpb, zp,
+        b_dW1, dtmph_sel, dtmp);
+
+    g_C<<<dim3(last ? 64 : 256), blk, 0, stream>>>(
+        dtmp, b_dW2, db2, dec, hnext, b_zpW, zpb, zp,
         phi_x + (size_t)(t + 1) * Bn * Hn, b_zeW1, zeb1, zepre,
         b_dW1, Cpre_dec, dtmph);
 
-    kS5<<<dim3(last ? 104 : 368), blk, 0, stream>>>(
+    g_D<<<dim3(last ? 104 : 368), blk, 0, stream>>>(
         dec, b_dmW, dmb, x + (size_t)t * Bn * Xn, out + 2,
         zepre, b_zeW2, zeb2, ze,
         zp, b_zpmW, zpmb, b_zpsW, zpsb, zpm, zps,
```

After: 7.281 ms. 10.6% more time.
